# Kernel tuning notes

Hardware: AMD Instinct MI355X
Metric: run time of the kernel (lower is better)

## Reference

```python
import jax, jax.numpy as jnp
import numpy as np
import math

B, S, D, H = 4, 2048, 1024, 16
DK = D // H


def setup_inputs() -> dict:
    key = jax.random.key(0)
    ks = jax.random.split(key, 12)
    scale = 1.0 / math.sqrt(D)
    inp = {
        "x": jax.random.normal(ks[0], (B, S, D), jnp.float32),
        "q": jax.random.normal(ks[1], (B, S, D), jnp.float32),
        "k": jax.random.normal(ks[2], (B, S, D), jnp.float32),
        "v": jax.random.normal(ks[3], (B, S, D), jnp.float32),
        # causal mask: 1 = keep, 0 = masked
        "mask": jnp.tril(jnp.ones((S, S), jnp.int32))[None, None],
        "wq": jax.random.normal(ks[4], (D, D), jnp.float32) * scale,
        "bq": jnp.zeros((D,), jnp.float32),
        "wk": jax.random.normal(ks[5], (D, D), jnp.float32) * scale,
        "bk": jnp.zeros((D,), jnp.float32),
        "wv": jax.random.normal(ks[6], (D, D), jnp.float32) * scale,
        "bv": jnp.zeros((D,), jnp.float32),
        "wo": jax.random.normal(ks[7], (D, D), jnp.float32) * scale,
        "bo": jnp.zeros((D,), jnp.float32),
    }
    return inp


def _split_heads(t):  # [B,S,D] -> [B,H,S,DK]
    return t.reshape(B, S, H, DK).transpose(0, 2, 1, 3)


def reference(x, q, k, v, mask, wq, bq, wk, bk, wv, bv, wo, bo):
    # x is accepted for signature parity with the torch module but is
    # overwritten inside the original forward; it does not affect output.
    query = _split_heads(q @ wq + bq)
    key_h = _split_heads(k @ wk + bk)
    value = _split_heads(v @ wv + bv)
    # scores: [B,H,Sq,Sk]
    scores = jnp.einsum("bhqd,bhkd->bhqk", query, key_h) / math.sqrt(DK)
    scores = jnp.where(mask == 0, jnp.float32(-1e9), scores)
    attn = jax.nn.softmax(scores, axis=-1)  # dropout p=0.0 -> identity
    out = jnp.einsum("bhqk,bhkd->bhqd", attn, value)
    out = out.transpose(0, 2, 1, 3).reshape(B, S, D)
    return out @ wo + bo
```

## Files before the change

kernel.cpp:

```cpp
#include <hip/hip_runtime.h>

typedef unsigned short u16;
typedef __bf16 bf16x8 __attribute__((ext_vector_type(8)));
typedef float f32x4 __attribute__((ext_vector_type(4)));
typedef u16 u16x8 __attribute__((ext_vector_type(8)));
typedef u16 u16x4 __attribute__((ext_vector_type(4)));

static constexpr int Bb = 4, Ss = 2048, Dd = 1024, Hh = 16, DKk = 64;
static constexpr int Mg = Bb * Ss;
static constexpr int Kg = Dd;
static constexpr int Ng = Dd;

#if __has_builtin(__builtin_amdgcn_exp2f)
#define EXP2 __builtin_amdgcn_exp2f
#else
#define EXP2 exp2f
#endif

__device__ __forceinline__ u16 f2b(float f) {
    union { __bf16 h; u16 u; } c; c.h = (__bf16)f; return c.u;
}

typedef const __attribute__((address_space(1))) void gas_t;
typedef __attribute__((address_space(3))) void las_t;
__device__ __forceinline__ void gll16(const void* g, void* l) {
    __builtin_amdgcn_global_load_lds((gas_t*)g, (las_t*)l, 16, 0, 0);
}

#define BARM  asm volatile("s_barrier" ::: "memory")
#define LGKM0 asm volatile("s_waitcnt lgkmcnt(0)" ::: "memory")
#define VMW(n) asm volatile("s_waitcnt vmcnt(" #n ")" ::: "memory")

__global__ __launch_bounds__(256) void conv3_kernel(const float* __restrict__ q,
                                                    const float* __restrict__ k,
                                                    const float* __restrict__ v,
                                                    u16* __restrict__ dst) {
    const size_t per = (size_t)Mg * Kg / 8;
    size_t id = (size_t)blockIdx.x * 256 + threadIdx.x;
    size_t t = id / per, off = (id % per) * 8;
    const float* src = (t == 0) ? q : (t == 1) ? k : v;
    float4 a = *(const float4*)(src + off);
    float4 b = *(const float4*)(src + off + 4);
    u16x8 o;
    o[0] = f2b(a.x); o[1] = f2b(a.y); o[2] = f2b(a.z); o[3] = f2b(a.w);
    o[4] = f2b(b.x); o[5] = f2b(b.y); o[6] = f2b(b.z); o[7] = f2b(b.w);
    *(u16x8*)(dst + t * (size_t)Mg * Kg + off) = o;
}

__global__ __launch_bounds__(256) void wt4_kernel(const float* w0, const float* w1,
                                                  const float* w2, const float* w3,
                                                  u16* t0, u16* t1, u16* t2, u16* t3) {
    const float* W; u16* Wt;
    switch (blockIdx.z) {
        case 0: W = w0; Wt = t0; break;
        case 1: W = w1; Wt = t1; break;
        case 2: W = w2; Wt = t2; break;
        default: W = w3; Wt = t3; break;
    }
    __shared__ __attribute__((aligned(16))) u16 T[64 * 72];
    const int k0 = blockIdx.x * 64, n0 = blockIdx.y * 64;
    const int tid = threadIdx.x;
    for (int i = 0; i < 4; ++i) {
        int flat = tid + i * 256;
        int r = flat >> 4, c4 = flat & 15;
        float4 w4 = *(const float4*)(W + (size_t)(k0 + r) * 1024 + n0 + c4 * 4);
        u16* d = &T[r * 72 + c4 * 4];
        d[0] = f2b(w4.x); d[1] = f2b(w4.y); d[2] = f2b(w4.z); d[3] = f2b(w4.w);
    }
    __syncthreads();
    for (int i = 0; i < 2; ++i) {
        int flat = tid + i * 256;
        int n = flat >> 3, c8 = flat & 7;
        u16x8 v;
        for (int jj = 0; jj < 8; ++jj) v[jj] = T[(c8 * 8 + jj) * 72 + n];
        *(u16x8*)(Wt + (size_t)(n0 + n) * 1024 + k0 + c8 * 8) = v;
    }
}

static constexpr int TILE = 256 * 64;
static constexpr int HALF = 128 * 64;

__device__ __forceinline__ void stage_half(const u16* s, u16* dst, int wave,
                                           int half, int kt) {
#pragma unroll
    for (int l = 0; l < 2; ++l) {
        const int c = wave * 2 + l;
        gll16(s + (size_t)(half * 128 + c * 8) * Kg + kt * 64, dst + c * 512);
    }
}

__device__ __forceinline__ void readA8(const u16* base, int wm, int mh,
                                       int l15, int quad, bf16x8* a) {
#pragma unroll
    for (int i = 0; i < 4; ++i) {
        const int row = wm * 128 + mh * 64 + i * 16 + l15;
        const u16* rp = base + row * 64;
        const int sw = row & 7;
        a[i * 2]     = *(const bf16x8*)(rp + ((quad)     ^ sw) * 8);
        a[i * 2 + 1] = *(const bf16x8*)(rp + ((quad + 4) ^ sw) * 8);
    }
}

__device__ __forceinline__ void readB4(const u16* base, int wn, int nh,
                                       int l15, int quad, bf16x8* b) {
#pragma unroll
    for (int j = 0; j < 2; ++j) {
        const int row = wn * 64 + nh * 32 + j * 16 + l15;
        const u16* rp = base + row * 64;
        const int sw = row & 7;
        b[j * 2]     = *(const bf16x8*)(rp + ((quad)     ^ sw) * 8);
        b[j * 2 + 1] = *(const bf16x8*)(rp + ((quad + 4) ^ sw) * 8);
    }
}

__device__ __forceinline__ void mfma16f(f32x4 (&acc)[8][4], int mh, int nh,
                                        const bf16x8* a, const bf16x8* b) {
    __builtin_amdgcn_s_setprio(1);
#pragma unroll
    for (int i = 0; i < 4; ++i)
#pragma unroll
        for (int j = 0; j < 2; ++j) {
            f32x4 c = acc[mh * 4 + i][nh * 2 + j];
            c = __builtin_amdgcn_mfma_f32_16x16x32_bf16(b[j * 2],     a[i * 2],     c, 0, 0, 0);
            c = __builtin_amdgcn_mfma_f32_16x16x32_bf16(b[j * 2 + 1], a[i * 2 + 1], c, 0, 0, 0);
            acc[mh * 4 + i][nh * 2 + j] = c;
        }
    __builtin_amdgcn_s_setprio(0);
}

__device__ __forceinline__ void gemm256_core(const u16* __restrict__ Asrc,
                                             const u16* __restrict__ Bsrc,
                                             u16* As, u16* Bs,
                                             f32x4 (&acc)[8][4]) {
    const int tid = threadIdx.x;
    const int wave = tid >> 6, lane = tid & 63;
    const int quad = lane >> 4, l15 = lane & 15;
    const int wm = wave >> 2, wn = wave & 3;
    const int r0 = lane >> 3, gsw = (lane & 7) ^ r0;
    const u16* sA = Asrc + (size_t)r0 * Kg + gsw * 8;
    const u16* sB = Bsrc + (size_t)r0 * Kg + gsw * 8;

    stage_half(sA, As + 0 * TILE + 0 * HALF, wave, 0, 0);
    stage_half(sA, As + 0 * TILE + 1 * HALF, wave, 1, 0);
    stage_half(sB, Bs + 0 * TILE + 0 * HALF, wave, 0, 0);
    stage_half(sB, Bs + 0 * TILE + 1 * HALF, wave, 1, 0);
    stage_half(sB, Bs + 1 * TILE + 0 * HALF, wave, 0, 1);
    stage_half(sB, Bs + 1 * TILE + 1 * HALF, wave, 1, 1);
    VMW(4); BARM;

    bf16x8 aF[8], b0F[4], b1F[4];
#pragma unroll 1
    for (int it = 0; it < 8; ++it) {
        const int t1 = 2 * it + 1;
        const int s2 = (2 * it + 2) & 15, s3 = (2 * it + 3) & 15;
        readA8(As + 0 * TILE, wm, 0, l15, quad, aF);
        readB4(Bs + 0 * TILE, wn, 0, l15, quad, b0F);
        stage_half(sA, As + 1 * TILE + 0 * HALF, wave, 0, t1);
        BARM; LGKM0;
        mfma16f(acc, 0, 0, aF, b0F);
        BARM;
        readB4(Bs + 0 * TILE, wn, 1, l15, quad, b1F);
        stage_half(sA, As + 1 * TILE + 1 * HALF, wave, 1, t1);
        BARM; LGKM0;
        mfma16f(acc, 0, 1, aF, b1F);
        BARM;
        readA8(As + 0 * TILE, wm, 1, l15, quad, aF);
        stage_half(sB, Bs + 0 * TILE + 0 * HALF, wave, 0, s2);
        BARM; LGKM0;
        mfma16f(acc, 1, 1, aF, b1F);
        BARM;
        stage_half(sB, Bs + 0 * TILE + 1 * HALF, wave, 1, s2);
        mfma16f(acc, 1, 0, aF, b0F);
        VMW(4); BARM;
        readA8(As + 1 * TILE, wm, 0, l15, quad, aF);
        readB4(Bs + 1 * TILE, wn, 0, l15, quad, b0F);
        stage_half(sA, As + 0 * TILE + 0 * HALF, wave, 0, s2);
        BARM; LGKM0;
        mfma16f(acc, 0, 0, aF, b0F);
        BARM;
        readB4(Bs + 1 * TILE, wn, 1, l15, quad, b1F);
        stage_half(sA, As + 0 * TILE + 1 * HALF, wave, 1, s2);
        BARM; LGKM0;
        mfma16f(acc, 0, 1, aF, b1F);
        BARM;
        readA8(As + 1 * TILE, wm, 1, l15, quad, aF);
        stage_half(sB, Bs + 1 * TILE + 0 * HALF, wave, 0, s3);
        BARM; LGKM0;
        mfma16f(acc, 1, 1, aF, b1F);
        BARM;
        stage_half(sB, Bs + 1 * TILE + 1 * HALF, wave, 1, s3);
        mfma16f(acc, 1, 0, aF, b0F);
        VMW(4); BARM;
    }
    VMW(0);
}

__global__ __launch_bounds__(512, 2) void qkv_gemm8(
    const u16* __restrict__ Ac,
    const u16* __restrict__ WqT, const u16* __restrict__ WkT,
    const u16* __restrict__ WvTw,
    const float* __restrict__ bq, const float* __restrict__ bk,
    const float* __restrict__ bv,
    u16* __restrict__ Qw, u16* __restrict__ Kw, u16* __restrict__ Vout,
    float qscale) {
    __shared__ __attribute__((aligned(16))) u16 As[2 * TILE];
    __shared__ __attribute__((aligned(16))) u16 Bs[2 * TILE];
    const int z = blockIdx.z;
    const int m0 = blockIdx.x * 256, n0 = blockIdx.y * 256;
    const u16* Asrc; const u16* Bsrc; const float* bias;
    if (z == 0)      { Asrc = Ac + (size_t)m0 * Kg;                    Bsrc = WqT + (size_t)n0 * Kg; bias = bq; }
    else if (z == 1) { Asrc = Ac + (size_t)Mg * Kg + (size_t)m0 * Kg;  Bsrc = WkT + (size_t)n0 * Kg; bias = bk; }
    else             { Asrc = WvTw + (size_t)n0 * Kg;                  Bsrc = Ac + (size_t)2 * Mg * Kg + (size_t)m0 * Kg; bias = bv; }

    f32x4 acc[8][4] = {};
    gemm256_core(Asrc, Bsrc, As, Bs, acc);

    const int tid = threadIdx.x, wave = tid >> 6, lane = tid & 63;
    const int quad = lane >> 4, l15 = lane & 15;
    const int wm = wave >> 2, wn = wave & 3;

    if (z < 2) {
        const float scale = (z == 0) ? qscale : 1.0f;
        u16* Out = (z == 0) ? Qw : Kw;
#pragma unroll
        for (int i = 0; i < 8; ++i) {
            const int m_row = m0 + wm * 128 + i * 16 + l15;
            const int bb = m_row >> 11, s = m_row & 2047;
#pragma unroll
            for (int j = 0; j < 4; ++j) {
                const int nb = n0 + wn * 64 + j * 16 + quad * 4;
                float4 b4 = *(const float4*)(bias + nb);
                const int h = nb >> 6, dk = nb & 63;
                u16x4 pk;
                pk[0] = f2b((acc[i][j][0] + b4.x) * scale);
                pk[1] = f2b((acc[i][j][1] + b4.y) * scale);
                pk[2] = f2b((acc[i][j][2] + b4.z) * scale);
                pk[3] = f2b((acc[i][j][3] + b4.w) * scale);
                *(u16x4*)(Out + (((size_t)bb * Hh + h) * Ss + s) * DKk + dk) = pk;
            }
        }
    } else {
#pragma unroll
        for (int i = 0; i < 8; ++i) {
            const int n = n0 + wm * 128 + i * 16 + l15;
            const int h = n >> 6, dk = n & 63;
            const float bvv = bias[n];
#pragma unroll
            for (int j = 0; j < 4; ++j) {
                const int mq = m0 + wn * 64 + j * 16 + quad * 4;
                const int bb = mq >> 11, s0 = mq & 2047;
                u16x4 pk;
#pragma unroll
                for (int r = 0; r < 4; ++r) pk[r] = f2b(acc[i][j][r] + bvv);
                *(u16x4*)(Vout + (((size_t)bb * Hh + h) * DKk + dk) * Ss + s0) = pk;
            }
        }
    }
}

__global__ __launch_bounds__(256) void out_gemm(const u16* __restrict__ A,
                                                const u16* __restrict__ Bt,
                                                const float* __restrict__ bias,
                                                float* __restrict__ Out) {
    __shared__ __attribute__((aligned(16))) u16 Asm[128 * 32];
    __shared__ __attribute__((aligned(16))) u16 Bsm[128 * 32];
    const int tid = threadIdx.x;
    const int wave = tid >> 6, lane = tid & 63;
    const int quad = lane >> 4, l15 = lane & 15;
    const int m0 = blockIdx.x * 128, n0 = blockIdx.y * 128;
    const int wm = (wave >> 1) * 64, wn = (wave & 1) * 64;
    const int rr = lane >> 2, cc = (lane & 3) * 8;

    const u16* Ag = A + (size_t)(m0 + wave * 32 + rr) * Kg + cc;
    const u16* Bg = Bt + (size_t)(n0 + wave * 32 + rr) * Kg + cc;
    u16* Asw = &Asm[wave * 32 * 32];
    u16* Bsw = &Bsm[wave * 32 * 32];

    f32x4 acc[4][4] = {};

    for (int k0 = 0; k0 < Kg; k0 += 32) {
        __syncthreads();
        gll16(Ag + k0, Asw);
        gll16(Ag + k0 + (size_t)16 * Kg, Asw + 16 * 32);
        gll16(Bg + k0, Bsw);
        gll16(Bg + k0 + (size_t)16 * Kg, Bsw + 16 * 32);
        __syncthreads();

        bf16x8 a[4], b[4];
        for (int i = 0; i < 4; ++i)
            a[i] = *(const bf16x8*)(&Asm[(wm + i * 16 + l15) * 32 + quad * 8]);
        for (int j = 0; j < 4; ++j)
            b[j] = *(const bf16x8*)(&Bsm[(wn + j * 16 + l15) * 32 + quad * 8]);
        for (int i = 0; i < 4; ++i)
            for (int j = 0; j < 4; ++j)
                acc[i][j] = __builtin_amdgcn_mfma_f32_16x16x32_bf16(b[j], a[i], acc[i][j], 0, 0, 0);
    }

    for (int i = 0; i < 4; ++i) {
        int m_row = m0 + wm + i * 16 + l15;
        for (int j = 0; j < 4; ++j) {
            int nb = n0 + wn + j * 16 + quad * 4;
            float4 b4 = *(const float4*)(bias + nb);
            float4 o;
            o.x = acc[i][j][0] + b4.x;
            o.y = acc[i][j][1] + b4.y;
            o.z = acc[i][j][2] + b4.z;
            o.w = acc[i][j][3] + b4.w;
            *(float4*)(Out + (size_t)m_row * Ng + nb) = o;
        }
    }
}

__global__ __launch_bounds__(256) void attn_kernel(const u16* __restrict__ Qw,
                                                   const u16* __restrict__ Kw,
                                                   const u16* __restrict__ Vt,
                                                   u16* __restrict__ Ow) {
    __shared__ __attribute__((aligned(16))) u16 QPs[4608];
    __shared__ __attribute__((aligned(16))) u16 Ks[4096];
    __shared__ __attribute__((aligned(16))) u16 Vs[4096];

    const int idx = blockIdx.x;
    const int qt = (Ss / 64 - 1) - (idx >> 6);
    const int bh = idx & 63;
    const int q0 = qt * 64;
    const int tid = threadIdx.x, wave = tid >> 6, lane = tid & 63;
    const int quad = lane >> 4, l15 = lane & 15;
    const int rr = lane >> 2, cc = (lane & 3) * 8;

    const u16* Qb = Qw + (size_t)bh * Ss * DKk;
    const u16* Kb = Kw + (size_t)bh * Ss * DKk;
    const u16* Vb = Vt + (size_t)bh * DKk * Ss;

    for (int kc = 0; kc < 2; ++kc)
        gll16(Qb + (size_t)(q0 + wave * 16 + rr) * DKk + kc * 32 + cc,
              &QPs[kc * 2048 + wave * 16 * 32]);
    __syncthreads();
    bf16x8 aq0 = *(const bf16x8*)(&QPs[(wave * 16 + l15) * 32 + quad * 8]);
    bf16x8 aq1 = *(const bf16x8*)(&QPs[2048 + (wave * 16 + l15) * 32 + quad * 8]);

    f32x4 acc_o[4] = {};
    float l_r = 0.f;
    const int qrow = q0 + wave * 16 + l15;
    u16* Pw = &QPs[wave * 1152];

    for (int j = 0; j <= qt; ++j) {
        __syncthreads();
        for (int c = 0; c < 2; ++c) {
            gll16(Kb + (size_t)(j * 64 + wave * 16 + rr) * DKk + c * 32 + cc,
                  &Ks[c * 2048 + wave * 16 * 32]);
            gll16(Vb + (size_t)(wave * 16 + rr) * Ss + j * 64 + c * 32 + cc,
                  &Vs[c * 2048 + wave * 16 * 32]);
        }
        __syncthreads();

        f32x4 sacc[4];
        for (int ct = 0; ct < 4; ++ct) {
            bf16x8 bk0 = *(const bf16x8*)(&Ks[(ct * 16 + l15) * 32 + quad * 8]);
            bf16x8 bk1 = *(const bf16x8*)(&Ks[2048 + (ct * 16 + l15) * 32 + quad * 8]);
            f32x4 z = {};
            z = __builtin_amdgcn_mfma_f32_16x16x32_bf16(bk0, aq0, z, 0, 0, 0);
            z = __builtin_amdgcn_mfma_f32_16x16x32_bf16(bk1, aq1, z, 0, 0, 0);
            sacc[ct] = z;
        }

        if (j == qt) {
            for (int ct = 0; ct < 4; ++ct) {
                int kbase = j * 64 + ct * 16 + quad * 4;
                for (int r = 0; r < 4; ++r)
                    if (kbase + r > qrow) sacc[ct][r] = -1e30f;
            }
        }

        const float M0 = 8.0f;
        float sum = 0.f;
        for (int ct = 0; ct < 4; ++ct)
            for (int r = 0; r < 4; ++r) {
                float p = EXP2(sacc[ct][r] - M0);
                sacc[ct][r] = p;
                sum += p;
            }
        l_r += sum;

        for (int ct = 0; ct < 4; ++ct) {
            u16x4 pk;
            for (int r = 0; r < 4; ++r) pk[r] = f2b(sacc[ct][r]);
            *(u16x4*)(&Pw[l15 * 72 + ct * 16 + quad * 4]) = pk;
        }

        for (int sc = 0; sc < 2; ++sc) {
            bf16x8 ap = *(const bf16x8*)(&Pw[l15 * 72 + sc * 32 + quad * 8]);
            for (int dt = 0; dt < 4; ++dt) {
                bf16x8 bv = *(const bf16x8*)(&Vs[sc * 2048 + (dt * 16 + l15) * 32 + quad * 8]);
                acc_o[dt] = __builtin_amdgcn_mfma_f32_16x16x32_bf16(bv, ap, acc_o[dt], 0, 0, 0);
            }
        }
    }

    const int b = bh >> 4, h = bh & 15;
    float L = l_r;
    L += __shfl_xor(L, 16, 64);
    L += __shfl_xor(L, 32, 64);
    const float inv = 1.f / L;
    const int s = q0 + wave * 16 + l15;
    u16* orow = Ow + (((size_t)b * Ss + s) * Hh + h) * DKk;
    for (int dt = 0; dt < 4; ++dt) {
        u16x4 pk;
        for (int r = 0; r < 4; ++r) pk[r] = f2b(acc_o[dt][r] * inv);
        *(u16x4*)(orow + dt * 16 + quad * 4) = pk;
    }
}

extern "C" void kernel_launch(void* const* d_in, const int* in_sizes, int n_in,
                              void* d_out, int out_size, void* d_ws, size_t ws_size,
                              hipStream_t stream) {
    const float* q  = (const float*)d_in[1];
    const float* k  = (const float*)d_in[2];
    const float* v  = (const float*)d_in[3];
    const float* wq = (const float*)d_in[5];
    const float* bq = (const float*)d_in[6];
    const float* wk = (const float*)d_in[7];
    const float* bk = (const float*)d_in[8];
    const float* wv = (const float*)d_in[9];
    const float* bv = (const float*)d_in[10];
    const float* wo = (const float*)d_in[11];
    const float* bo = (const float*)d_in[12];
    float* out = (float*)d_out;

    u16* WqT = (u16*)d_ws;
    u16* WkT = WqT + 1024 * 1024;
    u16* WvT = WkT + 1024 * 1024;
    u16* WoT = WvT + 1024 * 1024;
    u16* Ac  = WoT + 1024 * 1024;
    u16* Qw  = Ac + (size_t)3 * Mg * Kg;
    u16* Kw  = Qw + (size_t)Mg * Kg;
    u16* VwT = Kw + (size_t)Mg * Kg;
    u16* Ow  = Ac;

    conv3_kernel<<<dim3(3 * (Mg * Kg / 8) / 256), 256, 0, stream>>>(q, k, v, Ac);
    wt4_kernel<<<dim3(16, 16, 4), 256, 0, stream>>>(wq, wk, wv, wo, WqT, WkT, WvT, WoT);

    const float qscale = 0.125f * 1.44269504f;
    qkv_gemm8<<<dim3(Mg / 256, Ng / 256, 3), 512, 0, stream>>>(
        Ac, WqT, WkT, WvT, bq, bk, bv, Qw, Kw, VwT, qscale);

    attn_kernel<<<dim3(2048), 256, 0, stream>>>(Qw, Kw, VwT, Ow);

    out_gemm<<<dim3(Mg / 128, Ng / 128), 256, 0, stream>>>(Ow, WoT, bo, out);
}
```

Baseline: 349.1 us.

## Swizzle attention LDS tiles and pin GEMM LDS reads with inline asm

In the attention kernel, the Q, K and V shared-memory tiles now use an XOR swizzle on the 16-byte column chunk, applied both when global_load_lds writes them and when they are read for MFMA. The aim is to cut LDS bank conflicts on the 32-element-wide rows. In the QKV GEMM, the fragment reads become inline-asm ds_read_b128, and sched_barriers are added after each waitcnt so the compiler cannot reorder the MFMA blocks across them. The asm-volatile reads take the compiler's own scheduling and waitcnt tracking out of play, so correctness depends on the manual LGKM0 waits.

```diff
diff --git a/kernel.cpp b/kernel.cpp
--- a/kernel.cpp
+++ b/kernel.cpp
@@ -27,9 +27,18 @@
     __builtin_amdgcn_global_load_lds((gas_t*)g, (las_t*)l, 16, 0, 0);
 }
 
+__device__ __forceinline__ bf16x8 ldsrd(const u16* p) {
+    bf16x8 r;
+    asm volatile("ds_read_b128 %0, %1"
+                 : "=v"(r)
+                 : "v"((const __attribute__((address_space(3))) u16*)p));
+    return r;
+}
+
 #define BARM  asm volatile("s_barrier" ::: "memory")
 #define LGKM0 asm volatile("s_waitcnt lgkmcnt(0)" ::: "memory")
 #define VMW(n) asm volatile("s_waitcnt vmcnt(" #n ")" ::: "memory")
+#define SCHB  __builtin_amdgcn_sched_barrier(0)
 
 __global__ __launch_bounds__(256) void conv3_kernel(const float* __restrict__ q,
                                                     const float* __restrict__ k,
@@ -96,8 +105,8 @@
         const int row = wm * 128 + mh * 64 + i * 16 + l15;
         const u16* rp = base + row * 64;
         const int sw = row & 7;
-        a[i * 2]     = *(const bf16x8*)(rp + ((quad)     ^ sw) * 8);
-        a[i * 2 + 1] = *(const bf16x8*)(rp + ((quad + 4) ^ sw) * 8);
+        a[i * 2]     = ldsrd(rp + ((quad)     ^ sw) * 8);
+        a[i * 2 + 1] = ldsrd(rp + ((quad + 4) ^ sw) * 8);
     }
 }
 
@@ -108,8 +117,8 @@
         const int row = wn * 64 + nh * 32 + j * 16 + l15;
         const u16* rp = base + row * 64;
         const int sw = row & 7;
-        b[j * 2]     = *(const bf16x8*)(rp + ((quad)     ^ sw) * 8);
-        b[j * 2 + 1] = *(const bf16x8*)(rp + ((quad + 4) ^ sw) * 8);
+        b[j * 2]     = ldsrd(rp + ((quad)     ^ sw) * 8);
+        b[j * 2 + 1] = ldsrd(rp + ((quad + 4) ^ sw) * 8);
     }
 }
 
@@ -156,17 +165,17 @@
         readA8(As + 0 * TILE, wm, 0, l15, quad, aF);
         readB4(Bs + 0 * TILE, wn, 0, l15, quad, b0F);
         stage_half(sA, As + 1 * TILE + 0 * HALF, wave, 0, t1);
-        BARM; LGKM0;
+        BARM; LGKM0; SCHB;
         mfma16f(acc, 0, 0, aF, b0F);
         BARM;
         readB4(Bs + 0 * TILE, wn, 1, l15, quad, b1F);
         stage_half(sA, As + 1 * TILE + 1 * HALF, wave, 1, t1);
-        BARM; LGKM0;
+        BARM; LGKM0; SCHB;
         mfma16f(acc, 0, 1, aF, b1F);
         BARM;
         readA8(As + 0 * TILE, wm, 1, l15, quad, aF);
         stage_half(sB, Bs + 0 * TILE + 0 * HALF, wave, 0, s2);
-        BARM; LGKM0;
+        BARM; LGKM0; SCHB;
         mfma16f(acc, 1, 1, aF, b1F);
         BARM;
         stage_half(sB, Bs + 0 * TILE + 1 * HALF, wave, 1, s2);
@@ -175,17 +184,17 @@
         readA8(As + 1 * TILE, wm, 0, l15, quad, aF);
         readB4(Bs + 1 * TILE, wn, 0, l15, quad, b0F);
         stage_half(sA, As + 0 * TILE + 0 * HALF, wave, 0, s2);
-        BARM; LGKM0;
+        BARM; LGKM0; SCHB;
         mfma16f(acc, 0, 0, aF, b0F);
         BARM;
         readB4(Bs + 1 * TILE, wn, 1, l15, quad, b1F);
         stage_half(sA, As + 0 * TILE + 1 * HALF, wave, 1, s2);
-        BARM; LGKM0;
+        BARM; LGKM0; SCHB;
         mfma16f(acc, 0, 1, aF, b1F);
         BARM;
         readA8(As + 1 * TILE, wm, 1, l15, quad, aF);
         stage_half(sB, Bs + 1 * TILE + 0 * HALF, wave, 0, s3);
-        BARM; LGKM0;
+        BARM; LGKM0; SCHB;
         mfma16f(acc, 1, 1, aF, b1F);
         BARM;
         stage_half(sB, Bs + 1 * TILE + 1 * HALF, wave, 1, s3);
@@ -311,6 +320,8 @@
     }
 }
 
+__device__ __forceinline__ int swz4(int r) { return (r + (r >> 2)) & 3; }
+
 __global__ __launch_bounds__(256) void attn_kernel(const u16* __restrict__ Qw,
                                                    const u16* __restrict__ Kw,
                                                    const u16* __restrict__ Vt,
@@ -325,7 +336,9 @@
     const int q0 = qt * 64;
     const int tid = threadIdx.x, wave = tid >> 6, lane = tid & 63;
     const int quad = lane >> 4, l15 = lane & 15;
-    const int rr = lane >> 2, cc = (lane & 3) * 8;
+    const int rr = lane >> 2;
+    const int cc = (((lane & 3) ^ swz4(rr)) * 8);
+    const int hl = swz4(l15);
 
     const u16* Qb = Qw + (size_t)bh * Ss * DKk;
     const u16* Kb = Kw + (size_t)bh * Ss * DKk;
@@ -335,8 +348,8 @@
         gll16(Qb + (size_t)(q0 + wave * 16 + rr) * DKk + kc * 32 + cc,
               &QPs[kc * 2048 + wave * 16 * 32]);
     __syncthreads();
-    bf16x8 aq0 = *(const bf16x8*)(&QPs[(wave * 16 + l15) * 32 + quad * 8]);
-    bf16x8 aq1 = *(const bf16x8*)(&QPs[2048 + (wave * 16 + l15) * 32 + quad * 8]);
+    bf16x8 aq0 = *(const bf16x8*)(&QPs[(wave * 16 + l15) * 32 + (quad ^ hl) * 8]);
+    bf16x8 aq1 = *(const bf16x8*)(&QPs[2048 + (wave * 16 + l15) * 32 + (quad ^ hl) * 8]);
 
     f32x4 acc_o[4] = {};
     float l_r = 0.f;
@@ -355,8 +368,8 @@
 
         f32x4 sacc[4];
         for (int ct = 0; ct < 4; ++ct) {
-            bf16x8 bk0 = *(const bf16x8*)(&Ks[(ct * 16 + l15) * 32 + quad * 8]);
-            bf16x8 bk1 = *(const bf16x8*)(&Ks[2048 + (ct * 16 + l15) * 32 + quad * 8]);
+            bf16x8 bk0 = *(const bf16x8*)(&Ks[(ct * 16 + l15) * 32 + (quad ^ hl) * 8]);
+            bf16x8 bk1 = *(const bf16x8*)(&Ks[2048 + (ct * 16 + l15) * 32 + (quad ^ hl) * 8]);
             f32x4 z = {};
             z = __builtin_amdgcn_mfma_f32_16x16x32_bf16(bk0, aq0, z, 0, 0, 0);
             z = __builtin_amdgcn_mfma_f32_16x16x32_bf16(bk1, aq1, z, 0, 0, 0);
@@ -390,7 +403,7 @@
         for (int sc = 0; sc < 2; ++sc) {
             bf16x8 ap = *(const bf16x8*)(&Pw[l15 * 72 + sc * 32 + quad * 8]);
             for (int dt = 0; dt < 4; ++dt) {
-                bf16x8 bv = *(const bf16x8*)(&Vs[sc * 2048 + (dt * 16 + l15) * 32 + quad * 8]);
+                bf16x8 bv = *(const bf16x8*)(&Vs[sc * 2048 + (dt * 16 + l15) * 32 + (quad ^ hl) * 8]);
                 acc_o[dt] = __builtin_amdgcn_mfma_f32_16x16x32_bf16(bv, ap, acc_o[dt], 0, 0, 0);
             }
         }
```

After: 346.3 us. No clear change (-0.8%).
